# Optimization experiments

Measured on AMD Instinct MI355X. Metric: run time of the kernel, lower is better.

The kernel has to match this reference:

```python
import jax, jax.numpy as jnp
import numpy as np

B, S, L = 512, 150, 50          # batch, history length, prediction horizon
D, H, FF, NL = 128, 8, 256, 2   # d_model, heads, ffn hidden, encoder layers
DT = 0.1                        # self.dt


def _layernorm(x, g, b, eps=1e-5):
    mu = jnp.mean(x, axis=-1, keepdims=True)
    var = jnp.mean((x - mu) ** 2, axis=-1, keepdims=True)
    return (x - mu) / jnp.sqrt(var + eps) * g + b


def setup_inputs() -> dict:
    key = jax.random.key(0)
    ks = jax.random.split(key, 16)
    # inputs[:, :, :] = (position y, speed v, gap s, delta_v) over history
    pos = 100.0 * jax.random.uniform(ks[0], (B, S), jnp.float32)
    vel = 5.0 + 20.0 * jax.random.uniform(ks[1], (B, S), jnp.float32)
    gap = 10.0 + 30.0 * jax.random.uniform(ks[2], (B, S), jnp.float32)
    dvel = 0.5 * jax.random.normal(ks[3], (B, S), jnp.float32)
    inputs = jnp.stack([pos, vel, gap, dvel], axis=-1)
    # his_labels: leader position / speed over the horizon; keep leader ahead
    lead_y = inputs[:, -1, 0:1] + inputs[:, -1, 2:3] + 15.0 * jnp.arange(1, L + 1, dtype=jnp.float32)[None, :]
    lead_v = 15.0 + 2.0 * jax.random.uniform(ks[4], (B, L), jnp.float32)
    his_labels = jnp.stack([lead_y, lead_v], axis=-1)

    def u(k, shape, scale=0.05):
        return scale * jax.random.normal(k, shape, jnp.float32)

    params = dict(
        emb_w=u(ks[5], (D, 1)), emb_b=jnp.zeros((D,), jnp.float32),
        ipw=u(ks[6], (NL, 3 * D, D)), ipb=jnp.zeros((NL, 3 * D), jnp.float32),
        opw=u(ks[7], (NL, D, D)), opb=jnp.zeros((NL, D), jnp.float32),
        ln1g=jnp.ones((NL, D), jnp.float32), ln1b=jnp.zeros((NL, D), jnp.float32),
        l1w=u(ks[8], (NL, FF, D)), l1b=jnp.zeros((NL, FF), jnp.float32),
        l2w=u(ks[9], (NL, D, FF)), l2b=jnp.zeros((NL, D), jnp.float32),
        ln2g=jnp.ones((NL, D), jnp.float32), ln2b=jnp.zeros((NL, D), jnp.float32),
        dec_w=u(ks[10], (1, D)), dec_b=jnp.zeros((1,), jnp.float32),
        fus_w=u(ks[11], (1, 3)), fus_b=jnp.zeros((1,), jnp.float32),
    )
    return dict(inputs=inputs, his_labels=his_labels,
                s_0_input=jnp.float32(2.0), T_input=jnp.float32(1.5),
                a_input=jnp.float32(1.0), b_input=jnp.float32(1.5),
                v_d_input=jnp.float32(30.0), **params)


def _encoder_layer(x, mask, ipw, ipb, opw, opb, ln1g, ln1b, l1w, l1b, l2w, l2b, ln2g, ln2b):
    # x: [S, B, D]; torch post-norm TransformerEncoderLayer, relu, dropout=0
    Sq, Bb, Dd = x.shape
    dh = Dd // H
    qkv = x @ ipw.T + ipb                       # [S, B, 3D]
    q, k, v = jnp.split(qkv, 3, axis=-1)

    def heads(t):                               # [S, B, D] -> [B, H, S, dh]
        return t.reshape(Sq, Bb, H, dh).transpose(1, 2, 0, 3)

    q, k, v = heads(q), heads(k), heads(v)
    scores = jnp.einsum('bhqd,bhkd->bhqk', q, k) / jnp.sqrt(jnp.float32(dh)) + mask
    attn = jax.nn.softmax(scores, axis=-1)
    o = jnp.einsum('bhqk,bhkd->bhqd', attn, v).transpose(2, 0, 1, 3).reshape(Sq, Bb, Dd)
    o = o @ opw.T + opb
    x = _layernorm(x + o, ln1g, ln1b)
    ff = jax.nn.relu(x @ l1w.T + l1b) @ l2w.T + l2b
    return _layernorm(x + ff, ln2g, ln2b)


def _idm(inp_last, his, s0, T, a, b, vd, dt):
    # inp_last: [B, 4] = (y, v, s, delta_v); his: [B, L, 2] leader (y, v)
    y, v, s, dv = inp_last[:, 0], inp_last[:, 1], inp_last[:, 2], inp_last[:, 3]
    sq = 2.0 * jnp.sqrt(a * b)
    s_x = s0 + jnp.maximum(0.0, v * T + v * dv / sq)
    a_f = a * (1.0 - (v / vd) ** 4 - (s_x / s) ** 2)
    v0 = jnp.maximum(v + a_f * dt, 0.0)
    # NOTE: faithful to the torch source's bug: after the clipping loop the
    # loop variable i == B-1, so y_pred[:,0,0] = y + v_pred[B-1,0,0]*dt uses
    # the LAST batch element's speed for every row.
    y0 = y + v0[-1] * dt

    def step(carry, his_j):
        vj, yj = carry
        dvj = his_j[:, 1] - vj
        sj = his_j[:, 0] - yj
        sx = s0 + jnp.maximum(0.0, vj * T + vj * dvj / sq)
        acc = a * (1.0 - (vj / vd) ** 4 - (sx / sj) ** 2)
        v2 = vj + acc * dt
        v2 = jnp.where(v2 <= 0.0, 0.0, v2)
        y2 = yj + v2 * dt
        return (v2, y2), y2

    _, ys = jax.lax.scan(step, (v0, y0), his[:, :L - 1].transpose(1, 0, 2))  # ys: [L-1, B]
    y_pred = jnp.concatenate([y0[:, None], ys.T], axis=1)  # [B, L]
    return y_pred[:, :, None]


def reference(inputs, his_labels, s_0_input, T_input, a_input, b_input, v_d_input,
              emb_w, emb_b, ipw, ipb, opw, opb, ln1g, ln1b,
              l1w, l1b, l2w, l2b, ln2g, ln2b, dec_w, dec_b, fus_w, fus_b):
    src_in = inputs[:, :, 0:1]                               # [B, S, 1]
    src = src_in.transpose(1, 0, 2) @ emb_w.T + emb_b       # [S, B, D]
    mask = jnp.where(jnp.tril(jnp.ones((S, S), bool)), 0.0, -jnp.inf).astype(src.dtype)
    x = src
    for l in range(NL):
        x = _encoder_layer(x, mask, ipw[l], ipb[l], opw[l], opb[l],
                           ln1g[l], ln1b[l], l1w[l], l1b[l],
                           l2w[l], l2b[l], ln2g[l], ln2b[l])
    enc = x[-1]                                              # [B, D]
    out = jnp.broadcast_to(enc, (L, B, D)) @ dec_w.T + dec_b  # [L, B, 1]
    out = out.transpose(1, 0, 2)                             # [B, L, 1]
    # hist: per-row linspace(last, last + dv*L, L+1)[1:] == last + dv*(1..L)
    last = src_in[:, -1, 0]
    dvh = (last - src_in[:, -(1 + L), 0]) / L
    hist = (last[:, None] + dvh[:, None] * jnp.arange(1, L + 1, dtype=last.dtype))[:, :, None]
    y_idm = _idm(inputs[:, -1, :], his_labels, s_0_input, T_input,
                 a_input, b_input, v_d_input, DT)
    fusion = jnp.concatenate([out, hist, y_idm], axis=2)     # [B, L, 3]
    return fusion @ fus_w.T + fus_b                          # [B, L, 1]
```

## Files before the change

### kernel.cpp

```cpp
#include <hip/hip_runtime.h>

#define BB   512
#define SS   150
#define LL   50
#define DD   128
#define HH   8
#define DHH  16
#define FFD  256
#define NLL  2
#define MM   (SS*BB)
#define MDSZ ((size_t)MM*DD)
#define HREG 2400

typedef unsigned short u16;
typedef __attribute__((ext_vector_type(8))) short short8;
typedef __attribute__((ext_vector_type(4))) float f32x4;

__device__ __forceinline__ float bf2f(u16 u) {
    return __uint_as_float(((unsigned int)u) << 16);
}
__device__ __forceinline__ u16 f2bf(float f) {
    unsigned int x = __float_as_uint(f);
    unsigned int r = (x + 0x7fffu + ((x >> 16) & 1u)) >> 16;
    return (u16)r;
}
__device__ __forceinline__ float ldv(const void* p, size_t i, int bf) {
    return bf ? bf2f(((const u16*)p)[i]) : ((const float*)p)[i];
}
__device__ __forceinline__ float rd_scalar(const void* p) {
    const u16* q = (const u16*)p;
    u16 lo = q[0];
    if (lo != 0) return bf2f(lo);
    return *(const float*)p;
}
__device__ __forceinline__ f32x4 mfma16(short8 a, short8 b, f32x4 c) {
    return __builtin_amdgcn_mfma_f32_16x16x32_bf16(a, b, c, 0, 0, 0);
}
__device__ __forceinline__ float fexp2(float x) {
#if __has_builtin(__builtin_amdgcn_exp2f)
    return __builtin_amdgcn_exp2f(x);
#else
    return exp2f(x);
#endif
}
__device__ __forceinline__ float frcp(float x) {
#if __has_builtin(__builtin_amdgcn_rcpf)
    return __builtin_amdgcn_rcpf(x);
#else
    return 1.f / x;
#endif
}

__global__ void detect_kernel(const u16* __restrict__ ln1g, int* __restrict__ flag)
{
    *flag = (ln1g[0] == 0x3F80) ? 1 : 0;
}

#define WOFF_IPW 0
#define WOFF_OPW 98304
#define WOFF_L1W 131072
#define WOFF_L2W 196608
#define WTOTAL   262144
__global__ __launch_bounds__(256) void prep_kernel(
    const void* __restrict__ ipw, const void* __restrict__ opw,
    const void* __restrict__ l1w, const void* __restrict__ l2w,
    u16* __restrict__ wbf, const int* __restrict__ flag)
{
    int bf = *flag;
    int idx = blockIdx.x * 256 + threadIdx.x;
    if (idx >= WTOTAL) return;
    const void* src; size_t i;
    if (idx < WOFF_OPW)      { src = ipw; i = idx; }
    else if (idx < WOFF_L1W) { src = opw; i = idx - WOFF_OPW; }
    else if (idx < WOFF_L2W) { src = l1w; i = idx - WOFF_L1W; }
    else                     { src = l2w; i = idx - WOFF_L2W; }
    wbf[idx] = bf ? ((const u16*)src)[i] : f2bf(((const float*)src)[i]);
}

__global__ void prep2_kernel(
    const void* __restrict__ ipw, const void* __restrict__ ipb,
    const void* __restrict__ emb_w, const void* __restrict__ emb_b,
    float* __restrict__ uw, const int* __restrict__ flag)
{
    int bf = *flag;
    int c = threadIdx.x;
    float su = 0.f, sw = 0.f;
    for (int k = 0; k < DD; ++k) {
        float wv = ldv(ipw, (size_t)c * DD + k, bf);
        su += wv * ldv(emb_w, k, bf);
        sw += wv * ldv(emb_b, k, bf);
    }
    uw[c]       = su;
    uw[384 + c] = sw + ldv(ipb, c, bf);
}

__global__ __launch_bounds__(192) void attn0_kernel(
    const void* __restrict__ inputs, const float* __restrict__ uw,
    u16* __restrict__ o, const int* __restrict__ flag)
{
    __shared__ float pos_s[SS];
    __shared__ float pmax_s[SS];
    __shared__ float pmin_s[SS];

    int bid = blockIdx.x;
    int h = bid & 7, b = bid >> 3;
    int tid = threadIdx.x;
    int bf = *flag;

    if (tid < SS) pos_s[tid] = ldv(inputs, (size_t)(b * SS + tid) * 4 + 0, bf);
    __syncthreads();
    if (tid == 0) {
        float mx = pos_s[0], mn = pos_s[0];
        pmax_s[0] = mx; pmin_s[0] = mn;
        for (int t = 1; t < SS; ++t) {
            mx = fmaxf(mx, pos_s[t]); mn = fminf(mn, pos_s[t]);
            pmax_s[t] = mx; pmin_s[t] = mn;
        }
    }

    const float* uq = uw + h * 16;
    const float* wq = uw + 384 + h * 16;
    const float* uk = uw + 128 + h * 16;
    float A = 0.f, Bc = 0.f;
#pragma unroll
    for (int d = 0; d < 16; ++d) { A += uq[d] * uk[d]; Bc += wq[d] * uk[d]; }
    __syncthreads();

    int q = tid;
    if (q >= SS) return;
    float pq  = pos_s[q];
    const float L2E = 1.4426950408889634f;
    float cql = 0.25f * (pq * A + Bc) * L2E;
    float Ml  = fmaxf(cql * pmax_s[q], cql * pmin_s[q]);
    float s = 0.f, wsum = 0.f;
    for (int t = 0; t <= q; ++t) {
        float pt = pos_s[t];
        float e = fexp2(__builtin_fmaf(cql, pt, -Ml));
        s += e; wsum += e * pt;
    }
    float mq = wsum * frcp(s);

    const float* uv = uw + 256 + h * 16;
    const float* wv = uw + 384 + 256 + h * 16;
    u16 ov[16];
#pragma unroll
    for (int d = 0; d < 16; ++d) ov[d] = f2bf(mq * uv[d] + wv[d]);
    u16* dst = o + ((size_t)q * BB + b) * DD + h * DHH;
    *(uint4*)(dst)     = *(uint4*)(ov);
    *(uint4*)(dst + 8) = *(uint4*)(ov + 8);
}

#define LDPK 72
template<int EPI>
__global__ __launch_bounds__(256) void mfma_gemm(
    const u16* __restrict__ A, const u16* __restrict__ W,
    const void* __restrict__ bias, size_t boff,
    void* __restrict__ out, const u16* __restrict__ resid,
    int N, int K, const int* __restrict__ flag,
    const void* __restrict__ lng, const void* __restrict__ lnb, size_t goff,
    const void* __restrict__ ew, const void* __restrict__ eb)
{
    __shared__ __attribute__((aligned(16))) u16 As[64 * LDPK];
    __shared__ __attribute__((aligned(16))) u16 Bs[128 * LDPK];

    int bf = *flag;
    int tid  = threadIdx.x;
    int wave = tid >> 6, lane = tid & 63;
    int wy = wave >> 1, wx = wave & 1;
    int quad = lane >> 4, lr = lane & 15;
    int m0 = blockIdx.x * 64, n0 = blockIdx.y * 128;

    int aR = tid >> 2,          aC = (tid & 3) * 16;
    int bR0 = tid >> 2,         bC0 = (tid & 3) * 16;
    int bR1 = (tid + 256) >> 2, bC1 = (tid & 3) * 16;

    f32x4 acc[2][4] = {};

    for (int k0 = 0; k0 < K; k0 += 64) {
        const u16* ap  = A + (size_t)(m0 + aR) * K + k0 + aC;
        const u16* wp0 = W + (size_t)(n0 + bR0) * K + k0 + bC0;
        const u16* wp1 = W + (size_t)(n0 + bR1) * K + k0 + bC1;
        uint4 av0 = *(const uint4*)(ap);
        uint4 av1 = *(const uint4*)(ap + 8);
        uint4 w00 = *(const uint4*)(wp0);
        uint4 w01 = *(const uint4*)(wp0 + 8);
        uint4 w10 = *(const uint4*)(wp1);
        uint4 w11 = *(const uint4*)(wp1 + 8);
        __syncthreads();
        *(uint4*)(As + aR * LDPK + aC)       = av0;
        *(uint4*)(As + aR * LDPK + aC + 8)   = av1;
        *(uint4*)(Bs + bR0 * LDPK + bC0)     = w00;
        *(uint4*)(Bs + bR0 * LDPK + bC0 + 8) = w01;
        *(uint4*)(Bs + bR1 * LDPK + bC1)     = w10;
        *(uint4*)(Bs + bR1 * LDPK + bC1 + 8) = w11;
        __syncthreads();

#pragma unroll
        for (int ks = 0; ks < 64; ks += 32) {
            short8 a[2], b[4];
#pragma unroll
            for (int i = 0; i < 2; ++i)
                a[i] = *(const short8*)(As + (wy * 32 + i * 16 + lr) * LDPK + ks + quad * 8);
#pragma unroll
            for (int j = 0; j < 4; ++j)
                b[j] = *(const short8*)(Bs + (wx * 64 + j * 16 + lr) * LDPK + ks + quad * 8);
#pragma unroll
            for (int i = 0; i < 2; ++i)
#pragma unroll
                for (int j = 0; j < 4; ++j)
                    acc[i][j] = mfma16(a[i], b[j], acc[i][j]);
        }
    }

    if (EPI == 3 || EPI == 4) {
        float bvj[4];
#pragma unroll
        for (int j = 0; j < 4; ++j) bvj[j] = ldv(bias, boff + wx * 64 + j * 16 + lr, bf);

        float ewj[4], ebj[4], posr[2][4];
        if (EPI == 4) {
            int sblk  = m0 >> 9;
            int bbase = m0 & 511;
#pragma unroll
            for (int j = 0; j < 4; ++j) {
                int c = wx * 64 + j * 16 + lr;
                ewj[j] = ldv(ew, c, bf);
                ebj[j] = ldv(eb, c, bf);
            }
#pragma unroll
            for (int i = 0; i < 2; ++i)
#pragma unroll
                for (int r = 0; r < 4; ++r) {
                    int b = bbase + wy * 32 + i * 16 + quad * 4 + r;
                    posr[i][r] = ldv((const void*)resid, (size_t)(b * SS + sblk) * 4 + 0, bf);
                }
        }

        float s1[2][4] = {}, s2[2][4] = {};
#pragma unroll
        for (int j = 0; j < 4; ++j) {
            int c = wx * 64 + j * 16 + lr;
#pragma unroll
            for (int i = 0; i < 2; ++i)
#pragma unroll
                for (int r = 0; r < 4; ++r) {
                    int m = m0 + wy * 32 + i * 16 + quad * 4 + r;
                    float rv = (EPI == 4)
                               ? __builtin_fmaf(posr[i][r], ewj[j], ebj[j])
                               : bf2f(resid[(size_t)m * 128 + c]);
                    float v = acc[i][j][r] + bvj[j] + rv;
                    acc[i][j][r] = v;
                    s1[i][r] += v;
                    s2[i][r] += v * v;
                }
        }
#pragma unroll
        for (int i = 0; i < 2; ++i)
#pragma unroll
            for (int r = 0; r < 4; ++r)
#pragma unroll
                for (int msk = 1; msk < 16; msk <<= 1) {
                    s1[i][r] += __shfl_xor(s1[i][r], msk);
                    s2[i][r] += __shfl_xor(s2[i][r], msk);
                }

        __syncthreads();
        float* red = (float*)As;
        if (lr == 0) {
#pragma unroll
            for (int i = 0; i < 2; ++i)
#pragma unroll
                for (int r = 0; r < 4; ++r) {
                    int row = wy * 32 + i * 16 + quad * 4 + r;
                    red[wx * 128 + row]      = s1[i][r];
                    red[wx * 128 + 64 + row] = s2[i][r];
                }
        }
        __syncthreads();

        float gj[4], bj[4];
#pragma unroll
        for (int j = 0; j < 4; ++j) {
            int c = wx * 64 + j * 16 + lr;
            gj[j] = ldv(lng, goff + c, bf);
            bj[j] = ldv(lnb, goff + c, bf);
        }
#pragma unroll
        for (int i = 0; i < 2; ++i)
#pragma unroll
            for (int r = 0; r < 4; ++r) {
                int row = wy * 32 + i * 16 + quad * 4 + r;
                float t1 = red[row] + red[128 + row];
                float t2 = red[64 + row] + red[192 + row];
                float mu = t1 * (1.f / 128.f);
                float rstd = rsqrtf(t2 * (1.f / 128.f) - mu * mu + 1e-5f);
                size_t m = (size_t)(m0 + row);
#pragma unroll
                for (int j = 0; j < 4; ++j) {
                    int c = wx * 64 + j * 16 + lr;
                    ((u16*)out)[m * 128 + c] =
                        f2bf((acc[i][j][r] - mu) * rstd * gj[j] + bj[j]);
                }
            }
        return;
    }

    if (EPI == 2) {
        int sblk  = m0 >> 9;
        int bbase = m0 & 511;
#pragma unroll
        for (int j = 0; j < 4; ++j) {
            int c = n0 + wx * 64 + j * 16 + lr;
            float bvj = ldv(bias, boff + c, bf);
            int part = c >> 7;
            int hh   = (c >> 4) & 7;
#pragma unroll
            for (int i = 0; i < 2; ++i) {
#pragma unroll
                for (int r = 0; r < 4; ++r) {
                    int brow = bbase + wy * 32 + i * 16 + quad * 4 + r;
                    float v = acc[i][j][r] + bvj;
                    ((u16*)out)[((size_t)(brow * 8 + hh) * 3 + part) * HREG
                                + sblk * 16 + lr] = f2bf(v);
                }
            }
        }
        return;
    }

#pragma unroll
    for (int j = 0; j < 4; ++j) {
        int c = n0 + wx * 64 + j * 16 + lr;
        float bvj = ldv(bias, boff + c, bf);
#pragma unroll
        for (int i = 0; i < 2; ++i) {
#pragma unroll
            for (int r = 0; r < 4; ++r) {
                int m = m0 + wy * 32 + i * 16 + quad * 4 + r;
                float v = acc[i][j][r] + bvj;
                if (EPI == 1) v = fmaxf(v, 0.f);
                ((u16*)out)[(size_t)m * N + c] = f2bf(v);
            }
        }
    }
}

#define VSTR 168

template<int I, int PS>
__device__ __forceinline__ void attn_tile(
    short8 qf, int b, int h,
    const u16* K_lds, const u16* Vt_lds, u16* P_lds,
    u16* __restrict__ o, int lr, int quad)
{
    const f32x4 zz = {0.f, 0.f, 0.f, 0.f};

    f32x4 sc[I + 1];
#pragma unroll
    for (int jt = 0; jt <= I; ++jt) {
        int rr = 16 * jt + lr;
        short8 kf = *(const short8*)(K_lds + rr * 16 + (((quad & 1) ^ (lr & 1)) << 3));
        sc[jt] = mfma16(qf, kf, zz);
    }

    const float Cs = 0.36067376022224085f;
    float inv[4];
#pragma unroll
    for (int r = 0; r < 4; ++r) {
        int rg = 16 * I + quad * 4 + r;
        {
            int cg = 16 * I + lr;
            if (cg > rg) sc[I][r] = -3e38f;
        }
        float sm = 0.f;
#pragma unroll
        for (int jt = 0; jt <= I; ++jt) {
            float p = fexp2(sc[jt][r] * Cs);
            sm += p;
            P_lds[(quad * 4 + r) * PS + 16 * jt + lr] = f2bf(p);
        }
#pragma unroll
        for (int m = 1; m < 16; m <<= 1) sm += __shfl_xor(sm, m);
        inv[r] = frcp(sm);
    }

    constexpr int T   = I + 1;
    constexpr int NCH = (T + 1) / 2;
    f32x4 oa = zz;
#pragma unroll
    for (int ch = 0; ch < NCH; ++ch) {
        short8 pf = {};
        if (!((T & 1) && ch == NCH - 1 && quad >= 2))
            pf = *(const short8*)(P_lds + lr * PS + ch * 32 + quad * 8);
        short8 vf = *(const short8*)(Vt_lds + lr * VSTR + ch * 32 + quad * 8);
        oa = mfma16(pf, vf, oa);
    }
#pragma unroll
    for (int r = 0; r < 4; ++r) {
        int rg = 16 * I + quad * 4 + r;
        if (rg < SS)
            o[((size_t)rg * BB + b) * DD + h * DHH + lr] = f2bf(oa[r] * inv[r]);
    }
}

__global__ __launch_bounds__(512) void attn_kernel(
    const u16* __restrict__ qkv, u16* __restrict__ o)
{
    __shared__ __attribute__((aligned(16))) u16 K_lds[160 * 16];
    __shared__ __attribute__((aligned(16))) u16 Vt_lds[16 * VSTR];
    __shared__ __attribute__((aligned(16))) u16 P_lds[14336];

    int bid = blockIdx.x;
    int h = bid & 7;
    int b = bid >> 3;
    int tid = threadIdx.x;
    const u16* qbase = qkv + (size_t)bid * 3 * HREG;
    const u16* kbase = qbase + HREG;
    const u16* vbase = qbase + 2 * HREG;

    int wv = tid >> 6, lane = tid & 63;
    int quad = lane >> 4, lr = lane & 15;

    int t1 = (wv < 6) ? (9 - wv) : (wv == 6 ? 3 : 2);
    int t2 = (wv == 6) ? 0 : 1;

    short8 qf1 = {}, qf2 = {};
    {
        int q1 = 16 * t1 + lr;  if (q1 > SS - 1) q1 = SS - 1;
        int q2 = 16 * t2 + lr;
        if (quad < 2) {
            qf1 = *(const short8*)(qbase + q1 * 16 + quad * 8);
            if (wv >= 6)
                qf2 = *(const short8*)(qbase + q2 * 16 + quad * 8);
        }
    }

    u16* Vs = P_lds;
    if (tid < 320) {
        uint4 kv = {0u, 0u, 0u, 0u}, vv = {0u, 0u, 0u, 0u};
        int row, half;
        if (tid < 300) {
            row = tid >> 1; half = tid & 1;
            kv = *(const uint4*)(kbase + tid * 8);
            vv = *(const uint4*)(vbase + tid * 8);
        } else {
            row = 150 + ((tid - 300) >> 1); half = (tid - 300) & 1;
        }
        *(uint4*)(K_lds + row * 16 + ((half ^ (row & 1)) << 3)) = kv;
        *(uint4*)(Vs + row * 16 + (half << 3))                  = vv;
    }
    __syncthreads();
    for (int idx = tid; idx < 16 * 160; idx += 512) {
        int d = idx & 15, s = idx >> 4;
        Vt_lds[d * VSTR + s] = Vs[s * 16 + d];
    }
    __syncthreads();

    switch (wv) {
    case 0: attn_tile<9, 168>(qf1, b, h, K_lds, Vt_lds, P_lds +     0, o, lr, quad); break;
    case 1: attn_tile<8, 152>(qf1, b, h, K_lds, Vt_lds, P_lds +  2688, o, lr, quad); break;
    case 2: attn_tile<7, 136>(qf1, b, h, K_lds, Vt_lds, P_lds +  5120, o, lr, quad); break;
    case 3: attn_tile<6, 120>(qf1, b, h, K_lds, Vt_lds, P_lds +  7296, o, lr, quad); break;
    case 4: attn_tile<5, 104>(qf1, b, h, K_lds, Vt_lds, P_lds +  9216, o, lr, quad); break;
    case 5: attn_tile<4,  88>(qf1, b, h, K_lds, Vt_lds, P_lds + 10880, o, lr, quad); break;
    case 6: attn_tile<3,  72>(qf1, b, h, K_lds, Vt_lds, P_lds + 12288, o, lr, quad);
            attn_tile<0,  72>(qf2, b, h, K_lds, Vt_lds, P_lds + 12288, o, lr, quad); break;
    case 7: attn_tile<2,  56>(qf1, b, h, K_lds, Vt_lds, P_lds + 13440, o, lr, quad);
            attn_tile<1,  56>(qf2, b, h, K_lds, Vt_lds, P_lds + 13440, o, lr, quad); break;
    }
}

__global__ __launch_bounds__(64) void head_kernel(
    const u16* __restrict__ x, const void* __restrict__ inputs,
    const void* __restrict__ his,
    const void* s0p, const void* Tp, const void* ap, const void* bp, const void* vdp,
    const void* __restrict__ dec_w, const void* dec_b,
    const void* fus_w, const void* fus_b,
    void* __restrict__ out, const int* __restrict__ flag)
{
    int bf = *flag;
    int b = blockIdx.x * 64 + threadIdx.x;
    if (b >= BB) return;

    const u16* enc = x + ((size_t)((SS - 1) * BB + b)) * DD;
    float dot = 0.f;
    for (int d = 0; d < DD; ++d) dot += bf2f(enc[d]) * ldv(dec_w, d, bf);
    float outv = dot + ldv(dec_b, 0, bf);

    float last = ldv(inputs, (size_t)(b * SS + (SS - 1)) * 4 + 0, bf);
    float prev = ldv(inputs, (size_t)(b * SS + (SS - 1 - LL)) * 4 + 0, bf);
    float dvh = (last - prev) * (1.f / (float)LL);

    float s0 = rd_scalar(s0p), T = rd_scalar(Tp), a = rd_scalar(ap);
    float bb = rd_scalar(bp), vd = rd_scalar(vdp);
    float sq = 2.f * sqrtf(a * bb);
    const float dt = 0.1f;

    auto v0compute = [&](int bi) {
        size_t ip = (size_t)(bi * SS + (SS - 1)) * 4;
        float v  = ldv(inputs, ip + 1, bf);
        float s  = ldv(inputs, ip + 2, bf);
        float dv = ldv(inputs, ip + 3, bf);
        float sx = s0 + fmaxf(0.f, v * T + v * dv / sq);
        float r = v / vd, r2 = r * r;
        float rs = sx / s;
        float af = a * (1.f - r2 * r2 - rs * rs);
        return fmaxf(v + af * dt, 0.f);
    };
    float v0_last = v0compute(BB - 1);
    float v0      = v0compute(b);
    float y0 = last + v0_last * dt;

    float fw0 = ldv(fus_w, 0, bf), fw1 = ldv(fus_w, 1, bf), fw2 = ldv(fus_w, 2, bf);
    float fb  = ldv(fus_b, 0, bf);

    auto store = [&](int idx, float val) {
        if (bf) ((u16*)out)[idx] = f2bf(val);
        else    ((float*)out)[idx] = val;
    };

    store(b * LL + 0, fw0 * outv + fw1 * (last + dvh * 1.f) + fw2 * y0 + fb);

    float vj = v0, yj = y0;
    for (int j = 0; j < LL - 1; ++j) {
        float hy = ldv(his, (size_t)(b * LL + j) * 2 + 0, bf);
        float hv = ldv(his, (size_t)(b * LL + j) * 2 + 1, bf);
        float dvj = hv - vj;
        float sj  = hy - yj;
        float sx = s0 + fmaxf(0.f, vj * T + vj * dvj / sq);
        float r = vj / vd, r2 = r * r;
        float rs = sx / sj;
        float acc = a * (1.f - r2 * r2 - rs * rs);
        float v2 = vj + acc * dt;
        v2 = (v2 <= 0.f) ? 0.f : v2;
        float y2 = yj + v2 * dt;
        int l = j + 1;
        float histl = last + dvh * (float)(l + 1);
        store(b * LL + l, fw0 * outv + fw1 * histl + fw2 * y2 + fb);
        vj = v2; yj = y2;
    }
}

extern "C" void kernel_launch(void* const* d_in, const int* in_sizes, int n_in,
                              void* d_out, int out_size, void* d_ws, size_t ws_size,
                              hipStream_t stream)
{
    const void* inputs = d_in[0];
    const void* his    = d_in[1];
    const void* s0p    = d_in[2];
    const void* Tp     = d_in[3];
    const void* ap     = d_in[4];
    const void* bp     = d_in[5];
    const void* vdp    = d_in[6];
    const void* emb_w  = d_in[7];
    const void* emb_b  = d_in[8];
    const void* ipw    = d_in[9];
    const void* ipb    = d_in[10];
    const void* opw    = d_in[11];
    const void* opb    = d_in[12];
    const void* ln1g   = d_in[13];
    const void* ln1b   = d_in[14];
    const void* l1w    = d_in[15];
    const void* l1b    = d_in[16];
    const void* l2w    = d_in[17];
    const void* l2b    = d_in[18];
    const void* ln2g   = d_in[19];
    const void* ln2b   = d_in[20];
    const void* dec_w  = d_in[21];
    const void* dec_b  = d_in[22];
    const void* fus_w  = d_in[23];
    const void* fus_b  = d_in[24];

    u16*   wsu  = (u16*)d_ws;
    u16*   bx   = wsu;
    u16*   bqkv = wsu + 1 * MDSZ;
    u16*   bo   = wsu + 4 * MDSZ;
    u16*   h1   = wsu + 5 * MDSZ;
    u16*   wbf  = wsu + 7 * MDSZ;
    int*   flag = (int*)(wsu + 7 * MDSZ + WTOTAL);
    float* uw   = (float*)(wsu + 7 * MDSZ + WTOTAL + 2);

    detect_kernel<<<1, 1, 0, stream>>>((const u16*)ln1g, flag);
    prep_kernel<<<(WTOTAL + 255) / 256, 256, 0, stream>>>(ipw, opw, l1w, l2w, wbf, flag);
    prep2_kernel<<<1, 384, 0, stream>>>(ipw, ipb, emb_w, emb_b, uw, flag);

    for (int l = 0; l < NLL; ++l) {
        if (l == 0) {
            attn0_kernel<<<BB * HH, 192, 0, stream>>>(inputs, uw, bo, flag);
            mfma_gemm<4><<<dim3(MM / 64, 1), 256, 0, stream>>>(
                bo, wbf + WOFF_OPW, opb, 0,
                bx, (const u16*)inputs, 128, 128, flag, ln1g, ln1b, 0,
                emb_w, emb_b);
        } else {
            mfma_gemm<2><<<dim3(MM / 64, 3), 256, 0, stream>>>(
                bx, wbf + WOFF_IPW + (size_t)l * 384 * 128, ipb, (size_t)l * 384,
                bqkv, nullptr, 384, 128, flag, nullptr, nullptr, 0,
                nullptr, nullptr);
            attn_kernel<<<BB * HH, 512, 0, stream>>>(bqkv, bo);
            mfma_gemm<3><<<dim3(MM / 64, 1), 256, 0, stream>>>(
                bo, wbf + WOFF_OPW + (size_t)l * 128 * 128, opb, (size_t)l * 128,
                bx, bx, 128, 128, flag, ln1g, ln1b, (size_t)l * 128,
                nullptr, nullptr);
        }
        mfma_gemm<1><<<dim3(MM / 64, 2), 256, 0, stream>>>(
            bx, wbf + WOFF_L1W + (size_t)l * 256 * 128, l1b, (size_t)l * 256,
            h1, nullptr, 256, 128, flag, nullptr, nullptr, 0,
            nullptr, nullptr);
        mfma_gemm<3><<<dim3(MM / 64, 1), 256, 0, stream>>>(
            h1, wbf + WOFF_L2W + (size_t)l * 128 * 256, l2b, (size_t)l * 128,
            bx, bx, 128, 256, flag, ln2g, ln2b, (size_t)l * 128,
            nullptr, nullptr);
    }

    head_kernel<<<BB / 64, 64, 0, stream>>>(
        bx, inputs, his, s0p, Tp, ap, bp, vdp,
        dec_w, dec_b, fus_w, fus_b, d_out, flag);

    (void)in_sizes; (void)n_in; (void)out_size; (void)ws_size;
}
```

Measured before the change: 338.2 us.

## Compute only last timestep in final encoder layer

Since the head uses only the final timestep of the last encoder layer, layer 2 now computes K/V projections for all positions, Q only for the last 512 rows, attention for a single query per (batch, head), and out-proj/FFN/LN only on 512 rows. The full causal attention kernel is replaced by a simple single-query kernel. This removes most of layer 2's GEMM and attention work; it relies on the output depending only on x[-1], which holds for this model.

```diff
diff --git a/kernel.cpp b/kernel.cpp
--- a/kernel.cpp
+++ b/kernel.cpp
@@ -11,6 +11,7 @@
 #define MM   (SS*BB)
 #define MDSZ ((size_t)MM*DD)
 #define HREG 2400
+#define MLAST 76288
 
 typedef unsigned short u16;
 typedef __attribute__((ext_vector_type(8))) short short8;
@@ -158,7 +159,8 @@
     void* __restrict__ out, const u16* __restrict__ resid,
     int N, int K, const int* __restrict__ flag,
     const void* __restrict__ lng, const void* __restrict__ lnb, size_t goff,
-    const void* __restrict__ ew, const void* __restrict__ eb)
+    const void* __restrict__ ew, const void* __restrict__ eb,
+    int madd, int nadd)
 {
     __shared__ __attribute__((aligned(16))) u16 As[64 * LDPK];
     __shared__ __attribute__((aligned(16))) u16 Bs[128 * LDPK];
@@ -168,7 +170,7 @@
     int wave = tid >> 6, lane = tid & 63;
     int wy = wave >> 1, wx = wave & 1;
     int quad = lane >> 4, lr = lane & 15;
-    int m0 = blockIdx.x * 64, n0 = blockIdx.y * 128;
+    int m0 = blockIdx.x * 64, n0 = (blockIdx.y + nadd) * 128;
 
     int aR = tid >> 2,          aC = (tid & 3) * 16;
     int bR0 = tid >> 2,         bC0 = (tid & 3) * 16;
@@ -306,8 +308,9 @@
     }
 
     if (EPI == 2) {
-        int sblk  = m0 >> 9;
-        int bbase = m0 & 511;
+        int mglob = m0 + madd;
+        int sblk  = mglob >> 9;
+        int bbase = mglob & 511;
 #pragma unroll
         for (int j = 0; j < 4; ++j) {
             int c = n0 + wx * 64 + j * 16 + lr;
@@ -345,133 +348,83 @@
     }
 }
 
-#define VSTR 168
-
-template<int I, int PS>
-__device__ __forceinline__ void attn_tile(
-    short8 qf, int b, int h,
-    const u16* K_lds, const u16* Vt_lds, u16* P_lds,
-    u16* __restrict__ o, int lr, int quad)
-{
-    const f32x4 zz = {0.f, 0.f, 0.f, 0.f};
-
-    f32x4 sc[I + 1];
-#pragma unroll
-    for (int jt = 0; jt <= I; ++jt) {
-        int rr = 16 * jt + lr;
-        short8 kf = *(const short8*)(K_lds + rr * 16 + (((quad & 1) ^ (lr & 1)) << 3));
-        sc[jt] = mfma16(qf, kf, zz);
-    }
-
-    const float Cs = 0.36067376022224085f;
-    float inv[4];
-#pragma unroll
-    for (int r = 0; r < 4; ++r) {
-        int rg = 16 * I + quad * 4 + r;
-        {
-            int cg = 16 * I + lr;
-            if (cg > rg) sc[I][r] = -3e38f;
-        }
-        float sm = 0.f;
-#pragma unroll
-        for (int jt = 0; jt <= I; ++jt) {
-            float p = fexp2(sc[jt][r] * Cs);
-            sm += p;
-            P_lds[(quad * 4 + r) * PS + 16 * jt + lr] = f2bf(p);
-        }
-#pragma unroll
-        for (int m = 1; m < 16; m <<= 1) sm += __shfl_xor(sm, m);
-        inv[r] = frcp(sm);
-    }
-
-    constexpr int T   = I + 1;
-    constexpr int NCH = (T + 1) / 2;
-    f32x4 oa = zz;
-#pragma unroll
-    for (int ch = 0; ch < NCH; ++ch) {
-        short8 pf = {};
-        if (!((T & 1) && ch == NCH - 1 && quad >= 2))
-            pf = *(const short8*)(P_lds + lr * PS + ch * 32 + quad * 8);
-        short8 vf = *(const short8*)(Vt_lds + lr * VSTR + ch * 32 + quad * 8);
-        oa = mfma16(pf, vf, oa);
-    }
-#pragma unroll
-    for (int r = 0; r < 4; ++r) {
-        int rg = 16 * I + quad * 4 + r;
-        if (rg < SS)
-            o[((size_t)rg * BB + b) * DD + h * DHH + lr] = f2bf(oa[r] * inv[r]);
-    }
-}
-
-__global__ __launch_bounds__(512) void attn_kernel(
-    const u16* __restrict__ qkv, u16* __restrict__ o)
-{
-    __shared__ __attribute__((aligned(16))) u16 K_lds[160 * 16];
-    __shared__ __attribute__((aligned(16))) u16 Vt_lds[16 * VSTR];
-    __shared__ __attribute__((aligned(16))) u16 P_lds[14336];
-
+__global__ __launch_bounds__(64) void attn1_kernel(
+    const u16* __restrict__ qkv, u16* __restrict__ o1)
+{
     int bid = blockIdx.x;
-    int h = bid & 7;
-    int b = bid >> 3;
-    int tid = threadIdx.x;
+    int h = bid & 7, b = bid >> 3;
+    int lane = threadIdx.x;
     const u16* qbase = qkv + (size_t)bid * 3 * HREG;
     const u16* kbase = qbase + HREG;
     const u16* vbase = qbase + 2 * HREG;
 
-    int wv = tid >> 6, lane = tid & 63;
-    int quad = lane >> 4, lr = lane & 15;
-
-    int t1 = (wv < 6) ? (9 - wv) : (wv == 6 ? 3 : 2);
-    int t2 = (wv == 6) ? 0 : 1;
-
-    short8 qf1 = {}, qf2 = {};
+    float qv[16];
     {
-        int q1 = 16 * t1 + lr;  if (q1 > SS - 1) q1 = SS - 1;
-        int q2 = 16 * t2 + lr;
-        if (quad < 2) {
-            qf1 = *(const short8*)(qbase + q1 * 16 + quad * 8);
-            if (wv >= 6)
-                qf2 = *(const short8*)(qbase + q2 * 16 + quad * 8);
-        }
-    }
-
-    u16* Vs = P_lds;
-    if (tid < 320) {
-        uint4 kv = {0u, 0u, 0u, 0u}, vv = {0u, 0u, 0u, 0u};
-        int row, half;
-        if (tid < 300) {
-            row = tid >> 1; half = tid & 1;
-            kv = *(const uint4*)(kbase + tid * 8);
-            vv = *(const uint4*)(vbase + tid * 8);
-        } else {
-            row = 150 + ((tid - 300) >> 1); half = (tid - 300) & 1;
-        }
-        *(uint4*)(K_lds + row * 16 + ((half ^ (row & 1)) << 3)) = kv;
-        *(uint4*)(Vs + row * 16 + (half << 3))                  = vv;
-    }
-    __syncthreads();
-    for (int idx = tid; idx < 16 * 160; idx += 512) {
-        int d = idx & 15, s = idx >> 4;
-        Vt_lds[d * VSTR + s] = Vs[s * 16 + d];
-    }
-    __syncthreads();
-
-    switch (wv) {
-    case 0: attn_tile<9, 168>(qf1, b, h, K_lds, Vt_lds, P_lds +     0, o, lr, quad); break;
-    case 1: attn_tile<8, 152>(qf1, b, h, K_lds, Vt_lds, P_lds +  2688, o, lr, quad); break;
-    case 2: attn_tile<7, 136>(qf1, b, h, K_lds, Vt_lds, P_lds +  5120, o, lr, quad); break;
-    case 3: attn_tile<6, 120>(qf1, b, h, K_lds, Vt_lds, P_lds +  7296, o, lr, quad); break;
-    case 4: attn_tile<5, 104>(qf1, b, h, K_lds, Vt_lds, P_lds +  9216, o, lr, quad); break;
-    case 5: attn_tile<4,  88>(qf1, b, h, K_lds, Vt_lds, P_lds + 10880, o, lr, quad); break;
-    case 6: attn_tile<3,  72>(qf1, b, h, K_lds, Vt_lds, P_lds + 12288, o, lr, quad);
-            attn_tile<0,  72>(qf2, b, h, K_lds, Vt_lds, P_lds + 12288, o, lr, quad); break;
-    case 7: attn_tile<2,  56>(qf1, b, h, K_lds, Vt_lds, P_lds + 13440, o, lr, quad);
-            attn_tile<1,  56>(qf2, b, h, K_lds, Vt_lds, P_lds + 13440, o, lr, quad); break;
-    }
+        uint4 q0 = *(const uint4*)(qbase + 149 * 16);
+        uint4 q1 = *(const uint4*)(qbase + 149 * 16 + 8);
+        const unsigned int* qw = (const unsigned int*)&q0;
+#pragma unroll
+        for (int i = 0; i < 4; ++i) {
+            qv[2 * i]     = bf2f((u16)(qw[i] & 0xffff));
+            qv[2 * i + 1] = bf2f((u16)(qw[i] >> 16));
+        }
+        qw = (const unsigned int*)&q1;
+#pragma unroll
+        for (int i = 0; i < 4; ++i) {
+            qv[8 + 2 * i]     = bf2f((u16)(qw[i] & 0xffff));
+            qv[8 + 2 * i + 1] = bf2f((u16)(qw[i] >> 16));
+        }
+    }
+
+    const float Cs = 0.36067376022224085f;
+    float s = 0.f;
+    float ov[16] = {};
+    for (int t = lane; t < SS; t += 64) {
+        uint4 k0 = *(const uint4*)(kbase + t * 16);
+        uint4 k1 = *(const uint4*)(kbase + t * 16 + 8);
+        float dot = 0.f;
+        const unsigned int* kw = (const unsigned int*)&k0;
+#pragma unroll
+        for (int i = 0; i < 4; ++i) {
+            dot = __builtin_fmaf(qv[2 * i],     bf2f((u16)(kw[i] & 0xffff)), dot);
+            dot = __builtin_fmaf(qv[2 * i + 1], bf2f((u16)(kw[i] >> 16)),    dot);
+        }
+        kw = (const unsigned int*)&k1;
+#pragma unroll
+        for (int i = 0; i < 4; ++i) {
+            dot = __builtin_fmaf(qv[8 + 2 * i],     bf2f((u16)(kw[i] & 0xffff)), dot);
+            dot = __builtin_fmaf(qv[8 + 2 * i + 1], bf2f((u16)(kw[i] >> 16)),    dot);
+        }
+        float e = fexp2(dot * Cs);
+        s += e;
+        uint4 v0 = *(const uint4*)(vbase + t * 16);
+        uint4 v1 = *(const uint4*)(vbase + t * 16 + 8);
+        const unsigned int* vw = (const unsigned int*)&v0;
+#pragma unroll
+        for (int i = 0; i < 4; ++i) {
+            ov[2 * i]     = __builtin_fmaf(e, bf2f((u16)(vw[i] & 0xffff)), ov[2 * i]);
+            ov[2 * i + 1] = __builtin_fmaf(e, bf2f((u16)(vw[i] >> 16)),    ov[2 * i + 1]);
+        }
+        vw = (const unsigned int*)&v1;
+#pragma unroll
+        for (int i = 0; i < 4; ++i) {
+            ov[8 + 2 * i]     = __builtin_fmaf(e, bf2f((u16)(vw[i] & 0xffff)), ov[8 + 2 * i]);
+            ov[8 + 2 * i + 1] = __builtin_fmaf(e, bf2f((u16)(vw[i] >> 16)),    ov[8 + 2 * i + 1]);
+        }
+    }
+#pragma unroll
+    for (int msk = 1; msk < 64; msk <<= 1) {
+        s += __shfl_xor(s, msk);
+#pragma unroll
+        for (int d = 0; d < 16; ++d) ov[d] += __shfl_xor(ov[d], msk);
+    }
+    float inv = frcp(s);
+    if (lane < 16)
+        o1[(size_t)b * 128 + h * 16 + lane] = f2bf(ov[lane] * inv);
 }
 
 __global__ __launch_bounds__(64) void head_kernel(
-    const u16* __restrict__ x, const void* __restrict__ inputs,
+    const u16* __restrict__ xlast, const void* __restrict__ inputs,
     const void* __restrict__ his,
     const void* s0p, const void* Tp, const void* ap, const void* bp, const void* vdp,
     const void* __restrict__ dec_w, const void* dec_b,
@@ -482,7 +435,7 @@
     int b = blockIdx.x * 64 + threadIdx.x;
     if (b >= BB) return;
 
-    const u16* enc = x + ((size_t)((SS - 1) * BB + b)) * DD;
+    const u16* enc = xlast + (size_t)b * DD;
     float dot = 0.f;
     for (int d = 0; d < DD; ++d) dot += bf2f(enc[d]) * ldv(dec_w, d, bf);
     float outv = dot + ldv(dec_b, 0, bf);
@@ -579,41 +532,52 @@
     u16*   wbf  = wsu + 7 * MDSZ;
     int*   flag = (int*)(wsu + 7 * MDSZ + WTOTAL);
     float* uw   = (float*)(wsu + 7 * MDSZ + WTOTAL + 2);
+    u16*   o1   = bo;
+    u16*   y1   = bo + 512 * 128;
+    u16*   z1   = bo + 2 * 512 * 128;
 
     detect_kernel<<<1, 1, 0, stream>>>((const u16*)ln1g, flag);
     prep_kernel<<<(WTOTAL + 255) / 256, 256, 0, stream>>>(ipw, opw, l1w, l2w, wbf, flag);
     prep2_kernel<<<1, 384, 0, stream>>>(ipw, ipb, emb_w, emb_b, uw, flag);
 
-    for (int l = 0; l < NLL; ++l) {
-        if (l == 0) {
-            attn0_kernel<<<BB * HH, 192, 0, stream>>>(inputs, uw, bo, flag);
-            mfma_gemm<4><<<dim3(MM / 64, 1), 256, 0, stream>>>(
-                bo, wbf + WOFF_OPW, opb, 0,
-                bx, (const u16*)inputs, 128, 128, flag, ln1g, ln1b, 0,
-                emb_w, emb_b);
-        } else {
-            mfma_gemm<2><<<dim3(MM / 64, 3), 256, 0, stream>>>(
-                bx, wbf + WOFF_IPW + (size_t)l * 384 * 128, ipb, (size_t)l * 384,
-                bqkv, nullptr, 384, 128, flag, nullptr, nullptr, 0,
-                nullptr, nullptr);
-            attn_kernel<<<BB * HH, 512, 0, stream>>>(bqkv, bo);
-            mfma_gemm<3><<<dim3(MM / 64, 1), 256, 0, stream>>>(
-                bo, wbf + WOFF_OPW + (size_t)l * 128 * 128, opb, (size_t)l * 128,
-                bx, bx, 128, 128, flag, ln1g, ln1b, (size_t)l * 128,
-                nullptr, nullptr);
-        }
-        mfma_gemm<1><<<dim3(MM / 64, 2), 256, 0, stream>>>(
-            bx, wbf + WOFF_L1W + (size_t)l * 256 * 128, l1b, (size_t)l * 256,
-            h1, nullptr, 256, 128, flag, nullptr, nullptr, 0,
-            nullptr, nullptr);
-        mfma_gemm<3><<<dim3(MM / 64, 1), 256, 0, stream>>>(
-            h1, wbf + WOFF_L2W + (size_t)l * 128 * 256, l2b, (size_t)l * 128,
-            bx, bx, 128, 256, flag, ln2g, ln2b, (size_t)l * 128,
-            nullptr, nullptr);
-    }
+    attn0_kernel<<<BB * HH, 192, 0, stream>>>(inputs, uw, bo, flag);
+    mfma_gemm<4><<<dim3(MM / 64, 1), 256, 0, stream>>>(
+        bo, wbf + WOFF_OPW, opb, 0,
+        bx, (const u16*)inputs, 128, 128, flag, ln1g, ln1b, 0,
+        emb_w, emb_b, 0, 0);
+    mfma_gemm<1><<<dim3(MM / 64, 2), 256, 0, stream>>>(
+        bx, wbf + WOFF_L1W, l1b, 0,
+        h1, nullptr, 256, 128, flag, nullptr, nullptr, 0,
+        nullptr, nullptr, 0, 0);
+    mfma_gemm<3><<<dim3(MM / 64, 1), 256, 0, stream>>>(
+        h1, wbf + WOFF_L2W, l2b, 0,
+        bx, bx, 128, 256, flag, ln2g, ln2b, 0,
+        nullptr, nullptr, 0, 0);
+
+    mfma_gemm<2><<<dim3(MM / 64, 2), 256, 0, stream>>>(
+        bx, wbf + WOFF_IPW + (size_t)384 * 128, ipb, 384,
+        bqkv, nullptr, 384, 128, flag, nullptr, nullptr, 0,
+        nullptr, nullptr, 0, 1);
+    mfma_gemm<2><<<dim3(512 / 64, 1), 256, 0, stream>>>(
+        bx + (size_t)MLAST * 128, wbf + WOFF_IPW + (size_t)384 * 128, ipb, 384,
+        bqkv, nullptr, 384, 128, flag, nullptr, nullptr, 0,
+        nullptr, nullptr, MLAST, 0);
+    attn1_kernel<<<BB * HH, 64, 0, stream>>>(bqkv, o1);
+    mfma_gemm<3><<<dim3(512 / 64, 1), 256, 0, stream>>>(
+        o1, wbf + WOFF_OPW + (size_t)128 * 128, opb, 128,
+        y1, bx + (size_t)MLAST * 128, 128, 128, flag, ln1g, ln1b, 128,
+        nullptr, nullptr, 0, 0);
+    mfma_gemm<1><<<dim3(512 / 64, 2), 256, 0, stream>>>(
+        y1, wbf + WOFF_L1W + (size_t)256 * 128, l1b, 256,
+        h1, nullptr, 256, 128, flag, nullptr, nullptr, 0,
+        nullptr, nullptr, 0, 0);
+    mfma_gemm<3><<<dim3(512 / 64, 1), 256, 0, stream>>>(
+        h1, wbf + WOFF_L2W + (size_t)128 * 256, l2b, 128,
+        z1, y1, 128, 256, flag, ln2g, ln2b, 128,
+        nullptr, nullptr, 0, 0);
 
     head_kernel<<<BB / 64, 64, 0, stream>>>(
-        bx, inputs, his, s0p, Tp, ap, bp, vdp,
+        z1, inputs, his, s0p, Tp, ap, bp, vdp,
         dec_w, dec_b, fus_w, fus_b, d_out, flag);
 
     (void)in_sizes; (void)n_in; (void)out_size; (void)ws_size;
```

Result: faster. 297.1 us (-12.1%).
